# Kernel optimization log

Hardware: AMD Instinct MI355X
Metric: run time of the kernel (lower is better)

The kernel has to match this reference:

```python
import jax, jax.numpy as jnp
import numpy as np

DEPTH = 3
B, D, O = 8192, 1024, 1024
HR = 32            # router hidden
HE = 2 * D         # expert hidden
N_NODES = 2 ** DEPTH - 1
N_LEAVES = 2 ** DEPTH


def setup_inputs() -> dict:
    key = jax.random.key(0)
    ks = jax.random.split(key, 9)
    x = jax.random.normal(ks[0], (B, D), dtype=jnp.float32)
    # decision-node router params (stacked over nodes)
    rW1 = jax.random.normal(ks[1], (N_NODES, D, HR), dtype=jnp.float32) * 0.05
    rb1 = jnp.zeros((N_NODES, HR), dtype=jnp.float32)
    rW2 = jax.random.normal(ks[2], (N_NODES, HR, 2), dtype=jnp.float32) * 0.05
    rb2 = jnp.zeros((N_NODES, 2), dtype=jnp.float32)
    # leaf-expert params (stacked over experts)
    eW1 = jax.random.normal(ks[3], (N_LEAVES, D, HE), dtype=jnp.float32) * 0.02
    eb1 = jnp.zeros((N_LEAVES, HE), dtype=jnp.float32)
    eW2 = jax.random.normal(ks[4], (N_LEAVES, HE, O), dtype=jnp.float32) * 0.02
    eb2 = jnp.zeros((N_LEAVES, O), dtype=jnp.float32)
    return {"x": x, "rW1": rW1, "rb1": rb1, "rW2": rW2, "rb2": rb2,
            "eW1": eW1, "eb1": eb1, "eW2": eW2, "eb2": eb2, "top_k": 4}


def _gelu(v):
    return jax.nn.gelu(v, approximate=False)  # torch nn.GELU default = exact erf


def _leaf_probs(x, rW1, rb1, rW2, rb2):
    # all decision nodes batched: [N, B, 2]
    h = _gelu(jnp.einsum('bd,ndh->nbh', x, rW1) + rb1[:, None, :])
    logits = jnp.einsum('nbh,nhc->nbc', h, rW2) + rb2[:, None, :]
    dec = jax.nn.softmax(logits, axis=-1)
    # BFS product of path probabilities, level by level (fixed small loop)
    probs = jnp.ones((x.shape[0], 1), dtype=x.dtype)
    start = 0
    for level in range(DEPTH):
        w = 2 ** level
        dl = dec[start:start + w].transpose(1, 0, 2)       # [B, w, 2]
        probs = (probs[:, :, None] * dl).reshape(x.shape[0], 2 * w)
        start += w
    return probs  # [B, N_LEAVES]


def reference(x, rW1, rb1, rW2, rb2, eW1, eb1, eW2, eb2, top_k):
    leaf_probs = _leaf_probs(x, rW1, rb1, rW2, rb2)
    if top_k is not None and top_k < N_LEAVES:
        vals, idx = jax.lax.top_k(leaf_probs, top_k)       # [B, k]
        sparse = jnp.zeros_like(leaf_probs)
        sparse = sparse.at[jnp.arange(leaf_probs.shape[0])[:, None], idx].set(vals)
        leaf_probs = sparse / (sparse.sum(axis=1, keepdims=True) + 1e-8)
    # all leaf experts, batched (dense weighted sum; skip heuristic is an approximation)
    h = _gelu(jnp.einsum('bd,edh->ebh', x, eW1) + eb1[:, None, :])   # [E, B, HE]
    out = jnp.einsum('ebh,eho->ebo', h, eW2) + eb2[:, None, :]        # [E, B, O]
    y = jnp.einsum('ebo,be->bo', out, leaf_probs)
    return (y, leaf_probs)
```

## Files before the change

### kernel.cpp

```cpp
#include <hip/hip_runtime.h>
#include <hip/hip_bf16.h>
#include <cstdint>

#define B_   8192
#define D_   1024
#define O_   1024
#define HE_  2048
#define NN_  7
#define NL_  8
#define HR_  32
#define RC_  224
#define K3_  3072
#define MTMAX_ 264

typedef __attribute__((ext_vector_type(2))) float f32x2;
typedef __attribute__((ext_vector_type(4))) float f32x4;
typedef __attribute__((ext_vector_type(8))) short bf16x8;
typedef __attribute__((ext_vector_type(4))) unsigned short u16x4;
typedef unsigned short u16;
typedef unsigned int u32;

__device__ __forceinline__ u16 f2bf(float f) {
  __hip_bfloat16 h = __float2bfloat16(f);
  return *reinterpret_cast<u16*>(&h);
}
__device__ __forceinline__ float bf2f(u16 u) {
  u32 v = ((u32)u) << 16;
  return *reinterpret_cast<float*>(&v);
}
__device__ __forceinline__ float gelu_exact(float v) {
  return 0.5f * v * (1.0f + erff(v * 0.7071067811865475f));
}
__device__ __forceinline__ void gload16(const void* g, void* l) {
  __builtin_amdgcn_global_load_lds(
      (const __attribute__((address_space(1))) void*)(uintptr_t)g,
      (__attribute__((address_space(3))) void*)(uintptr_t)l,
      16, 0, 0);
}

__global__ __launch_bounds__(256) void build_xbs_kernel(
    const float* __restrict__ in, u16* __restrict__ out) {
  size_t i = ((size_t)blockIdx.x * 256 + threadIdx.x) * 4;
  size_t row = i >> 10;
  int col = (int)(i & 1023);
  f32x4 f = *reinterpret_cast<const f32x4*>(in + i);
  u16x4 hi, lo;
#pragma unroll
  for (int j = 0; j < 4; j++) {
    hi[j] = f2bf(f[j]);
    lo[j] = f2bf(f[j] - bf2f(hi[j]));
  }
  u16* base = out + row * 2048 + col;
  *reinterpret_cast<u16x4*>(base)        = hi;
  *reinterpret_cast<u16x4*>(base + 1024) = lo;
}

__global__ __launch_bounds__(256) void build_wr3_kernel(
    const float* __restrict__ rW1, u16* __restrict__ Wr3) {
  size_t i = ((size_t)blockIdx.x * 256 + threadIdx.x) * 4;
  int c = (int)(i / K3_), k = (int)(i % K3_);
  int j = k >> 10, kk = k & 1023;
  u16x4 o;
  if (c < RC_) {
    int node = c >> 5, h = c & 31;
    const float* src = rW1 + ((size_t)node * 1024 + kk) * HR_ + h;
#pragma unroll
    for (int t = 0; t < 4; t++) {
      float f = src[t * HR_];
      u16 hi = f2bf(f);
      o[t] = (j == 1) ? f2bf(f - bf2f(hi)) : hi;
    }
  } else {
    o[0] = 0; o[1] = 0; o[2] = 0; o[3] = 0;
  }
  *reinterpret_cast<u16x4*>(Wr3 + i) = o;
}

__global__ __launch_bounds__(256) void transpose_cvt_kernel(
    const float* __restrict__ in, u16* __restrict__ out,
    int R, int C, int ldo, long in_estride, long out_estride) {
  __shared__ __attribute__((aligned(16))) float tile[64][65];
  const float* in_e = in + (long)blockIdx.z * in_estride;
  u16* out_e = out + (long)blockIdx.z * out_estride;
  int t = threadIdx.x;
  int r0 = blockIdx.y * 64, c0 = blockIdx.x * 64;
  int cc = t & 63, rbase = t >> 6;
#pragma unroll
  for (int i = 0; i < 16; i++) {
    int rr = rbase + i * 4;
    tile[rr][cc] = in_e[(long)(r0 + rr) * C + c0 + cc];
  }
  __syncthreads();
  int r2 = (t & 31) * 2, cj = t >> 5;
#pragma unroll
  for (int i = 0; i < 8; i++) {
    int c = cj * 8 + i;
    u32 u = (u32)f2bf(tile[r2][c]) | ((u32)f2bf(tile[r2 + 1][c]) << 16);
    *reinterpret_cast<u32*>(out_e + (long)(c0 + c) * ldo + r0 + r2) = u;
  }
}

__global__ __launch_bounds__(256, 2) void router_gemm_kernel(
    const u16* __restrict__ Xbs, const u16* __restrict__ Bm,
    float* __restrict__ H1p) {
  __shared__ __attribute__((aligned(16))) u16 lA[128 * 32];
  __shared__ __attribute__((aligned(16))) u16 lB[128 * 32];
  int tid = threadIdx.x;
  int gid = blockIdx.x;
  int cpx = gridDim.x >> 3;
  gid = (gid & 7) * cpx + (gid >> 3);
  int s = gid >> 7;
  int rem = gid & 127;
  int band = rem >> 4, inb = rem & 15;
  long m0 = (long)(band * 8 + (inb & 7)) * 128;
  long n0 = (long)(inb >> 3) * 128;
  int wid = tid >> 6, lane = tid & 63;
  int wm = wid >> 1, wn = wid & 1;
  f32x4 acc[4][4];
#pragma unroll
  for (int m = 0; m < 4; m++)
#pragma unroll
    for (int n = 0; n < 4; n++) acc[m][n] = (f32x4){0.f, 0.f, 0.f, 0.f};
  int lr = lane & 15, lk = (lane >> 4) * 8;
  int srow = tid >> 2, soff = (tid & 3) * 8;
  const u16* Bb = Bm + n0 * K3_;
  int kbeg = s * 768, kend = kbeg + 768;
  for (int k0 = kbeg; k0 < kend; k0 += 32) {
    int ca = (k0 < 1024) ? k0 : k0 - 1024;
    gload16(Xbs + (m0 + srow) * 2048 + ca + soff, &lA[tid * 8]);
    gload16(Xbs + (m0 + 64 + srow) * 2048 + ca + soff, &lA[(256 + tid) * 8]);
    gload16(Bb + (long)srow * K3_ + k0 + soff, &lB[tid * 8]);
    gload16(Bb + (long)(64 + srow) * K3_ + k0 + soff, &lB[(256 + tid) * 8]);
    __syncthreads();
    bf16x8 af[4], bfr[4];
#pragma unroll
    for (int m = 0; m < 4; m++)
      af[m] = *reinterpret_cast<const bf16x8*>(&lA[(wm * 64 + m * 16 + lr) * 32 + lk]);
#pragma unroll
    for (int n = 0; n < 4; n++)
      bfr[n] = *reinterpret_cast<const bf16x8*>(&lB[(wn * 64 + n * 16 + lr) * 32 + lk]);
#pragma unroll
    for (int m = 0; m < 4; m++)
#pragma unroll
      for (int n = 0; n < 4; n++)
        acc[m][n] = __builtin_amdgcn_mfma_f32_16x16x32_bf16(af[m], bfr[n], acc[m][n], 0, 0, 0);
    __syncthreads();
  }
  int lq = lane >> 4;
#pragma unroll
  for (int m = 0; m < 4; m++)
#pragma unroll
    for (int n = 0; n < 4; n++)
#pragma unroll
      for (int j = 0; j < 4; j++) {
        long row = m0 + wm * 64 + m * 16 + lq * 4 + j;
        long col = n0 + wn * 64 + n * 16 + lr;
        if (col < RC_)
          H1p[((long)s * B_ + row) * RC_ + col] = acc[m][n][j];
      }
}

__global__ __launch_bounds__(256) void router_logits_kernel(
    const float* __restrict__ H1p, const float* __restrict__ rb1,
    const float* __restrict__ rW2, const float* __restrict__ rb2,
    const int* __restrict__ topk_ptr, float* __restrict__ P) {
  int b = blockIdx.x * 256 + threadIdx.x;
  float dec[NN_][2];
#pragma unroll
  for (int n = 0; n < NN_; n++) {
    float l0 = rb2[n * 2], l1 = rb2[n * 2 + 1];
#pragma unroll
    for (int r4 = 0; r4 < HR_; r4 += 4) {
      int c = n * HR_ + r4;
      f32x4 hs = *reinterpret_cast<const f32x4*>(&H1p[((long)0 * B_ + b) * RC_ + c]);
#pragma unroll
      for (int s = 1; s < 4; s++)
        hs += *reinterpret_cast<const f32x4*>(&H1p[((long)s * B_ + b) * RC_ + c]);
      f32x4 bv = *reinterpret_cast<const f32x4*>(rb1 + c);
#pragma unroll
      for (int j = 0; j < 4; j++) {
        float hv = gelu_exact(hs[j] + bv[j]);
        l0 += hv * rW2[(c + j) * 2];
        l1 += hv * rW2[(c + j) * 2 + 1];
      }
    }
    float mx = fmaxf(l0, l1);
    float e0 = expf(l0 - mx), e1 = expf(l1 - mx);
    float sm = e0 + e1;
    dec[n][0] = e0 / sm; dec[n][1] = e1 / sm;
  }
  float v[NL_];
#pragma unroll
  for (int L = 0; L < NL_; L++)
    v[L] = dec[0][L >> 2] * dec[1 + (L >> 2)][(L >> 1) & 1] * dec[3 + (L >> 1)][L & 1];
  int tk = *topk_ptr;
  float p[NL_];
  if (tk < NL_) {
    float s = 0.f;
    bool keep[NL_];
#pragma unroll
    for (int e = 0; e < NL_; e++) {
      int rank = 0;
#pragma unroll
      for (int j = 0; j < NL_; j++)
        rank += ((v[j] > v[e]) || (v[j] == v[e] && j < e)) ? 1 : 0;
      keep[e] = rank < tk;
      if (keep[e]) s += v[e];
    }
    float inv = 1.f / (s + 1e-8f);
#pragma unroll
    for (int e = 0; e < NL_; e++) p[e] = keep[e] ? v[e] * inv : 0.f;
  } else {
#pragma unroll
    for (int e = 0; e < NL_; e++) p[e] = v[e];
  }
#pragma unroll
  for (int e = 0; e < NL_; e++) P[(long)b * NL_ + e] = p[e];
}

__global__ __launch_bounds__(256) void yinit_kernel(
    const float* __restrict__ P, const float* __restrict__ eb2,
    float* __restrict__ y) {
  size_t i = ((size_t)blockIdx.x * 256 + threadIdx.x) * 4;
  size_t row = i >> 10;
  int col = (int)(i & 1023);
  f32x4 s = (f32x4){0.f, 0.f, 0.f, 0.f};
#pragma unroll
  for (int e = 0; e < NL_; e++) {
    float pe = P[row * NL_ + e];
    f32x4 w = *reinterpret_cast<const f32x4*>(eb2 + (size_t)e * O_ + col);
    s += w * pe;
  }
  *reinterpret_cast<f32x4*>(y + i) = s;
}

__global__ __launch_bounds__(256) void compact_kernel(
    const float* __restrict__ P, int* __restrict__ idx,
    int* __restrict__ counts) {
  int e = blockIdx.x, t = threadIdx.x;
  __shared__ int sc[256];
  __shared__ int sbase;
  if (t == 0) sbase = 0;
  __syncthreads();
  for (int c0 = 0; c0 < B_; c0 += 256) {
    int r = c0 + t;
    int f = (P[(long)r * NL_ + e] > 0.f) ? 1 : 0;
    sc[t] = f;
    __syncthreads();
#pragma unroll
    for (int d = 1; d < 256; d <<= 1) {
      int v = (t >= d) ? sc[t - d] : 0;
      __syncthreads();
      sc[t] += v;
      __syncthreads();
    }
    int pos = sbase + sc[t] - 1;
    int tot = sc[255];
    if (f) idx[(long)e * B_ + pos] = r;
    __syncthreads();
    if (t == 0) sbase += tot;
    __syncthreads();
  }
  if (t == 0) counts[e] = sbase;
}

__global__ void tiles_kernel(const int* __restrict__ counts,
                             int* __restrict__ toff) {
  int s = 0;
#pragma unroll
  for (int e = 0; e < NL_; e++) { toff[e] = s; s += (counts[e] + 127) >> 7; }
  toff[NL_] = s;
}

__global__ __launch_bounds__(256, 2) void gemme1_kernel(
    const u16* __restrict__ Xbs, const u16* __restrict__ W1t,
    const float* __restrict__ eb1, const float* __restrict__ P,
    u16* __restrict__ Hall, const int* __restrict__ idx,
    const int* __restrict__ counts, const int* __restrict__ toff) {
  __shared__ __attribute__((aligned(16))) u16 lA[128 * 32];
  __shared__ __attribute__((aligned(16))) u16 lB[128 * 32];
  int tid = threadIdx.x;
  int gid = blockIdx.x;
  int cpx = gridDim.x >> 3;
  gid = (gid & 7) * cpx + (gid >> 3);
  int mt = gid >> 4, nt = gid & 15;
  if (mt >= toff[NL_]) return;
  int e = 0;
#pragma unroll
  for (int f = 1; f < NL_; f++) e += (mt >= toff[f]) ? 1 : 0;
  int cnt = counts[e];
  long m0 = (long)(mt - toff[e]) * 128;
  long n0 = (long)nt * 128;
  const int* idxe = idx + (long)e * B_;
  int wid = tid >> 6, lane = tid & 63;
  int wm = wid >> 1, wn = wid & 1;
  f32x4 acc[4][4];
#pragma unroll
  for (int m = 0; m < 4; m++)
#pragma unroll
    for (int n = 0; n < 4; n++) acc[m][n] = (f32x4){0.f, 0.f, 0.f, 0.f};
  int lr = lane & 15, lk = (lane >> 4) * 8;
  int srow = tid >> 2, soff = (tid & 3) * 8;
  int gi0 = (m0 + srow < cnt) ? idxe[m0 + srow] : 0;
  int gi1 = (m0 + 64 + srow < cnt) ? idxe[m0 + 64 + srow] : 0;
  const u16* ar0 = Xbs + (long)gi0 * 2048;
  const u16* ar1 = Xbs + (long)gi1 * 2048;
  const u16* Bb = W1t + ((size_t)e * HE_ + n0) * D_;
  for (int k0 = 0; k0 < D_; k0 += 32) {
    gload16(ar0 + k0 + soff, &lA[tid * 8]);
    gload16(ar1 + k0 + soff, &lA[(256 + tid) * 8]);
    gload16(Bb + (long)srow * D_ + k0 + soff, &lB[tid * 8]);
    gload16(Bb + (long)(64 + srow) * D_ + k0 + soff, &lB[(256 + tid) * 8]);
    __syncthreads();
    bf16x8 af[4], bfr[4];
#pragma unroll
    for (int m = 0; m < 4; m++)
      af[m] = *reinterpret_cast<const bf16x8*>(&lA[(wm * 64 + m * 16 + lr) * 32 + lk]);
#pragma unroll
    for (int n = 0; n < 4; n++)
      bfr[n] = *reinterpret_cast<const bf16x8*>(&lB[(wn * 64 + n * 16 + lr) * 32 + lk]);
#pragma unroll
    for (int m = 0; m < 4; m++)
#pragma unroll
      for (int n = 0; n < 4; n++)
        acc[m][n] = __builtin_amdgcn_mfma_f32_16x16x32_bf16(af[m], bfr[n], acc[m][n], 0, 0, 0);
    __syncthreads();
  }
  int lq = lane >> 4;
  long hbase = (long)toff[e] * 128;
#pragma unroll
  for (int m = 0; m < 4; m++) {
#pragma unroll
    for (int j = 0; j < 4; j++) {
      long lrow = m0 + wm * 64 + m * 16 + lq * 4 + j;
      if (lrow >= cnt) continue;
      int orow = idxe[lrow];
      float pw = P[(long)orow * NL_ + e];
#pragma unroll
      for (int n = 0; n < 4; n++) {
        long col = n0 + wn * 64 + n * 16 + lr;
        float g = gelu_exact(acc[m][n][j] + eb1[(size_t)e * HE_ + col]);
        Hall[(hbase + lrow) * HE_ + col] = f2bf(g * pw);
      }
    }
  }
}

__global__ __launch_bounds__(256, 2) void gemme2_kernel(
    const u16* __restrict__ Hall, const u16* __restrict__ W2t,
    float* __restrict__ y, const int* __restrict__ idx,
    const int* __restrict__ counts, const int* __restrict__ toff) {
  __shared__ __attribute__((aligned(16))) u16 lA[128 * 32];
  __shared__ __attribute__((aligned(16))) u16 lB[128 * 32];
  int tid = threadIdx.x;
  int gid = blockIdx.x;
  int cpx = gridDim.x >> 3;
  gid = (gid & 7) * cpx + (gid >> 3);
  int mt = gid >> 3, nt = gid & 7;
  if (mt >= toff[NL_]) return;
  int e = 0;
#pragma unroll
  for (int f = 1; f < NL_; f++) e += (mt >= toff[f]) ? 1 : 0;
  int cnt = counts[e];
  long m0 = (long)(mt - toff[e]) * 128;
  long n0 = (long)nt * 128;
  const int* idxe = idx + (long)e * B_;
  int wid = tid >> 6, lane = tid & 63;
  int wm = wid >> 1, wn = wid & 1;
  f32x4 acc[4][4];
#pragma unroll
  for (int m = 0; m < 4; m++)
#pragma unroll
    for (int n = 0; n < 4; n++) acc[m][n] = (f32x4){0.f, 0.f, 0.f, 0.f};
  int lr = lane & 15, lk = (lane >> 4) * 8;
  int srow = tid >> 2, soff = (tid & 3) * 8;
  const u16* Ab = Hall + ((long)toff[e] * 128 + m0) * HE_;
  const u16* Bb = W2t + n0 * ((size_t)NL_ * HE_) + (size_t)e * HE_;
  for (int k0 = 0; k0 < HE_; k0 += 32) {
    gload16(Ab + (long)srow * HE_ + k0 + soff, &lA[tid * 8]);
    gload16(Ab + (long)(64 + srow) * HE_ + k0 + soff, &lA[(256 + tid) * 8]);
    gload16(Bb + (size_t)srow * (NL_ * HE_) + k0 + soff, &lB[tid * 8]);
    gload16(Bb + (size_t)(64 + srow) * (NL_ * HE_) + k0 + soff, &lB[(256 + tid) * 8]);
    __syncthreads();
    bf16x8 af[4], bfr[4];
#pragma unroll
    for (int m = 0; m < 4; m++)
      af[m] = *reinterpret_cast<const bf16x8*>(&lA[(wm * 64 + m * 16 + lr) * 32 + lk]);
#pragma unroll
    for (int n = 0; n < 4; n++)
      bfr[n] = *reinterpret_cast<const bf16x8*>(&lB[(wn * 64 + n * 16 + lr) * 32 + lk]);
#pragma unroll
    for (int m = 0; m < 4; m++)
#pragma unroll
      for (int n = 0; n < 4; n++)
        acc[m][n] = __builtin_amdgcn_mfma_f32_16x16x32_bf16(af[m], bfr[n], acc[m][n], 0, 0, 0);
    __syncthreads();
  }
  int lq = lane >> 4;
#pragma unroll
  for (int m = 0; m < 4; m++) {
#pragma unroll
    for (int j = 0; j < 4; j++) {
      long lrow = m0 + wm * 64 + m * 16 + lq * 4 + j;
      if (lrow >= cnt) continue;
      long orow = idxe[lrow];
#pragma unroll
      for (int n = 0; n < 4; n++) {
        long col = n0 + wn * 64 + n * 16 + lr;
        unsafeAtomicAdd(&y[orow * O_ + col], acc[m][n][j]);
      }
    }
  }
}

extern "C" void kernel_launch(void* const* d_in, const int* in_sizes, int n_in,
                              void* d_out, int out_size, void* d_ws, size_t ws_size,
                              hipStream_t stream) {
  (void)in_sizes; (void)n_in; (void)out_size; (void)ws_size;
  const float* x   = (const float*)d_in[0];
  const float* rW1 = (const float*)d_in[1];
  const float* rb1 = (const float*)d_in[2];
  const float* rW2 = (const float*)d_in[3];
  const float* rb2 = (const float*)d_in[4];
  const float* eW1 = (const float*)d_in[5];
  const float* eb1 = (const float*)d_in[6];
  const float* eW2 = (const float*)d_in[7];
  const float* eb2 = (const float*)d_in[8];
  const int*  topk = (const int*)d_in[9];
  float* y = (float*)d_out;
  float* P = y + (size_t)B_ * O_;

  char* ws = (char*)d_ws;
  u16*  Xbs = (u16*)ws;
  u16*  W1t = (u16*)(ws + 33554432);
  u16*  W2t = (u16*)(ws + 67108864);
  int*  idx    = (int*)(ws + 100663296);
  int*  counts = (int*)(ws + 100925440);
  int*  toff   = (int*)(ws + 100925504);
  char* hreg   = ws + 100925952;
  u16*  Hall = (u16*)hreg;
  u16*  Wr3  = (u16*)hreg;
  float* H1p = (float*)(hreg + 2097152);

  build_xbs_kernel<<<(B_ * D_) / 1024, 256, 0, stream>>>(x, Xbs);
  build_wr3_kernel<<<(256 * K3_) / 1024, 256, 0, stream>>>(rW1, Wr3);
  transpose_cvt_kernel<<<dim3(HE_ / 64, D_ / 64, NL_), 256, 0, stream>>>(
      eW1, W1t, D_, HE_, D_, (long)D_ * HE_, (long)HE_ * D_);
  transpose_cvt_kernel<<<dim3(O_ / 64, HE_ / 64, NL_), 256, 0, stream>>>(
      eW2, W2t, HE_, O_, NL_ * HE_, (long)HE_ * O_, (long)HE_);
  router_gemm_kernel<<<512, 256, 0, stream>>>(Xbs, Wr3, H1p);
  router_logits_kernel<<<B_ / 256, 256, 0, stream>>>(H1p, rb1, rW2, rb2, topk, P);
  yinit_kernel<<<(B_ * O_) / 1024, 256, 0, stream>>>(P, eb2, y);
  compact_kernel<<<NL_, 256, 0, stream>>>(P, idx, counts);
  tiles_kernel<<<1, 1, 0, stream>>>(counts, toff);

  gemme1_kernel<<<MTMAX_ * 16, 256, 0, stream>>>(
      Xbs, W1t, eb1, P, Hall, idx, counts, toff);
  gemme2_kernel<<<MTMAX_ * 8, 256, 0, stream>>>(
      Hall, W2t, y, idx, counts, toff);
}
```

Measured before the change: 721.8 us.

## Deepen expert GEMM K-tile to 64 with XOR-swizzled LDS and per-expert W2 layout

```diff
diff --git a/kernel.cpp b/kernel.cpp
--- a/kernel.cpp
+++ b/kernel.cpp
@@ -277,8 +277,8 @@
     const float* __restrict__ eb1, const float* __restrict__ P,
     u16* __restrict__ Hall, const int* __restrict__ idx,
     const int* __restrict__ counts, const int* __restrict__ toff) {
-  __shared__ __attribute__((aligned(16))) u16 lA[128 * 32];
-  __shared__ __attribute__((aligned(16))) u16 lB[128 * 32];
+  __shared__ __attribute__((aligned(16))) u16 lA[128 * 64];
+  __shared__ __attribute__((aligned(16))) u16 lB[128 * 64];
   int tid = threadIdx.x;
   int gid = blockIdx.x;
   int cpx = gridDim.x >> 3;
@@ -299,31 +299,60 @@
   for (int m = 0; m < 4; m++)
 #pragma unroll
     for (int n = 0; n < 4; n++) acc[m][n] = (f32x4){0.f, 0.f, 0.f, 0.f};
-  int lr = lane & 15, lk = (lane >> 4) * 8;
-  int srow = tid >> 2, soff = (tid & 3) * 8;
-  int gi0 = (m0 + srow < cnt) ? idxe[m0 + srow] : 0;
-  int gi1 = (m0 + 64 + srow < cnt) ? idxe[m0 + 64 + srow] : 0;
-  const u16* ar0 = Xbs + (long)gi0 * 2048;
-  const u16* ar1 = Xbs + (long)gi1 * 2048;
+  int lr = lane & 15, lkg = lane >> 4;
+  const u16* gA[4]; const u16* gB[4]; int lds_o[4];
   const u16* Bb = W1t + ((size_t)e * HE_ + n0) * D_;
-  for (int k0 = 0; k0 < D_; k0 += 32) {
-    gload16(ar0 + k0 + soff, &lA[tid * 8]);
-    gload16(ar1 + k0 + soff, &lA[(256 + tid) * 8]);
-    gload16(Bb + (long)srow * D_ + k0 + soff, &lB[tid * 8]);
-    gload16(Bb + (long)(64 + srow) * D_ + k0 + soff, &lB[(256 + tid) * 8]);
-    __syncthreads();
-    bf16x8 af[4], bfr[4];
+#pragma unroll
+  for (int i = 0; i < 4; i++) {
+    int sidx = tid + i * 256;
+    int r = sidx >> 3, j = sidx & 7;
+    int so = ((j ^ (r & 7)) << 3);
+    int gi = (m0 + r < cnt) ? idxe[m0 + r] : 0;
+    gA[i] = Xbs + (long)gi * 2048 + so;
+    gB[i] = Bb + (long)r * D_ + so;
+    lds_o[i] = sidx * 8;
+  }
+  int foA[4][2], foB[4][2];
+#pragma unroll
+  for (int m = 0; m < 4; m++) {
+    int r = wm * 64 + m * 16 + lr;
+#pragma unroll
+    for (int kk = 0; kk < 2; kk++)
+      foA[m][kk] = r * 128 + ((((kk * 4 + lkg) ^ (r & 7))) << 4);
+  }
+#pragma unroll
+  for (int n = 0; n < 4; n++) {
+    int r = wn * 64 + n * 16 + lr;
+#pragma unroll
+    for (int kk = 0; kk < 2; kk++)
+      foB[n][kk] = r * 128 + ((((kk * 4 + lkg) ^ (r & 7))) << 4);
+  }
+  const char* pa = (const char*)lA;
+  const char* pb = (const char*)lB;
+  for (int k0 = 0; k0 < D_; k0 += 64) {
+#pragma unroll
+    for (int i = 0; i < 4; i++) gload16(gA[i] + k0, &lA[lds_o[i]]);
+#pragma unroll
+    for (int i = 0; i < 4; i++) gload16(gB[i] + k0, &lB[lds_o[i]]);
+    __syncthreads();
+    bf16x8 af[4][2], bfr[4][2];
+#pragma unroll
+    for (int m = 0; m < 4; m++) {
+      af[m][0] = *reinterpret_cast<const bf16x8*>(pa + foA[m][0]);
+      af[m][1] = *reinterpret_cast<const bf16x8*>(pa + foA[m][1]);
+    }
+#pragma unroll
+    for (int n = 0; n < 4; n++) {
+      bfr[n][0] = *reinterpret_cast<const bf16x8*>(pb + foB[n][0]);
+      bfr[n][1] = *reinterpret_cast<const bf16x8*>(pb + foB[n][1]);
+    }
 #pragma unroll
     for (int m = 0; m < 4; m++)
-      af[m] = *reinterpret_cast<const bf16x8*>(&lA[(wm * 64 + m * 16 + lr) * 32 + lk]);
-#pragma unroll
-    for (int n = 0; n < 4; n++)
-      bfr[n] = *reinterpret_cast<const bf16x8*>(&lB[(wn * 64 + n * 16 + lr) * 32 + lk]);
-#pragma unroll
-    for (int m = 0; m < 4; m++)
-#pragma unroll
-      for (int n = 0; n < 4; n++)
-        acc[m][n] = __builtin_amdgcn_mfma_f32_16x16x32_bf16(af[m], bfr[n], acc[m][n], 0, 0, 0);
+#pragma unroll
+      for (int n = 0; n < 4; n++) {
+        acc[m][n] = __builtin_amdgcn_mfma_f32_16x16x32_bf16(af[m][0], bfr[n][0], acc[m][n], 0, 0, 0);
+        acc[m][n] = __builtin_amdgcn_mfma_f32_16x16x32_bf16(af[m][1], bfr[n][1], acc[m][n], 0, 0, 0);
+      }
     __syncthreads();
   }
   int lq = lane >> 4;
@@ -350,8 +379,8 @@
     const u16* __restrict__ Hall, const u16* __restrict__ W2t,
     float* __restrict__ y, const int* __restrict__ idx,
     const int* __restrict__ counts, const int* __restrict__ toff) {
-  __shared__ __attribute__((aligned(16))) u16 lA[128 * 32];
-  __shared__ __attribute__((aligned(16))) u16 lB[128 * 32];
+  __shared__ __attribute__((aligned(16))) u16 lA[128 * 64];
+  __shared__ __attribute__((aligned(16))) u16 lB[128 * 64];
   int tid = threadIdx.x;
   int gid = blockIdx.x;
   int cpx = gridDim.x >> 3;
@@ -372,28 +401,60 @@
   for (int m = 0; m < 4; m++)
 #pragma unroll
     for (int n = 0; n < 4; n++) acc[m][n] = (f32x4){0.f, 0.f, 0.f, 0.f};
-  int lr = lane & 15, lk = (lane >> 4) * 8;
-  int srow = tid >> 2, soff = (tid & 3) * 8;
+  int lr = lane & 15, lkg = lane >> 4;
   const u16* Ab = Hall + ((long)toff[e] * 128 + m0) * HE_;
-  const u16* Bb = W2t + n0 * ((size_t)NL_ * HE_) + (size_t)e * HE_;
-  for (int k0 = 0; k0 < HE_; k0 += 32) {
-    gload16(Ab + (long)srow * HE_ + k0 + soff, &lA[tid * 8]);
-    gload16(Ab + (long)(64 + srow) * HE_ + k0 + soff, &lA[(256 + tid) * 8]);
-    gload16(Bb + (size_t)srow * (NL_ * HE_) + k0 + soff, &lB[tid * 8]);
-    gload16(Bb + (size_t)(64 + srow) * (NL_ * HE_) + k0 + soff, &lB[(256 + tid) * 8]);
-    __syncthreads();
-    bf16x8 af[4], bfr[4];
+  const u16* Bb = W2t + ((size_t)e * O_ + n0) * HE_;
+  const u16* gA[4]; const u16* gB[4]; int lds_o[4];
+#pragma unroll
+  for (int i = 0; i < 4; i++) {
+    int sidx = tid + i * 256;
+    int r = sidx >> 3, j = sidx & 7;
+    int so = ((j ^ (r & 7)) << 3);
+    gA[i] = Ab + (long)r * HE_ + so;
+    gB[i] = Bb + (long)r * HE_ + so;
+    lds_o[i] = sidx * 8;
+  }
+  int foA[4][2], foB[4][2];
+#pragma unroll
+  for (int m = 0; m < 4; m++) {
+    int r = wm * 64 + m * 16 + lr;
+#pragma unroll
+    for (int kk = 0; kk < 2; kk++)
+      foA[m][kk] = r * 128 + ((((kk * 4 + lkg) ^ (r & 7))) << 4);
+  }
+#pragma unroll
+  for (int n = 0; n < 4; n++) {
+    int r = wn * 64 + n * 16 + lr;
+#pragma unroll
+    for (int kk = 0; kk < 2; kk++)
+      foB[n][kk] = r * 128 + ((((kk * 4 + lkg) ^ (r & 7))) << 4);
+  }
+  const char* pa = (const char*)lA;
+  const char* pb = (const char*)lB;
+  for (int k0 = 0; k0 < HE_; k0 += 64) {
+#pragma unroll
+    for (int i = 0; i < 4; i++) gload16(gA[i] + k0, &lA[lds_o[i]]);
+#pragma unroll
+    for (int i = 0; i < 4; i++) gload16(gB[i] + k0, &lB[lds_o[i]]);
+    __syncthreads();
+    bf16x8 af[4][2], bfr[4][2];
+#pragma unroll
+    for (int m = 0; m < 4; m++) {
+      af[m][0] = *reinterpret_cast<const bf16x8*>(pa + foA[m][0]);
+      af[m][1] = *reinterpret_cast<const bf16x8*>(pa + foA[m][1]);
+    }
+#pragma unroll
+    for (int n = 0; n < 4; n++) {
+      bfr[n][0] = *reinterpret_cast<const bf16x8*>(pb + foB[n][0]);
+      bfr[n][1] = *reinterpret_cast<const bf16x8*>(pb + foB[n][1]);
+    }
 #pragma unroll
     for (int m = 0; m < 4; m++)
-      af[m] = *reinterpret_cast<const bf16x8*>(&lA[(wm * 64 + m * 16 + lr) * 32 + lk]);
-#pragma unroll
-    for (int n = 0; n < 4; n++)
-      bfr[n] = *reinterpret_cast<const bf16x8*>(&lB[(wn * 64 + n * 16 + lr) * 32 + lk]);
-#pragma unroll
-    for (int m = 0; m < 4; m++)
-#pragma unroll
-      for (int n = 0; n < 4; n++)
-        acc[m][n] = __builtin_amdgcn_mfma_f32_16x16x32_bf16(af[m], bfr[n], acc[m][n], 0, 0, 0);
+#pragma unroll
+      for (int n = 0; n < 4; n++) {
+        acc[m][n] = __builtin_amdgcn_mfma_f32_16x16x32_bf16(af[m][0], bfr[n][0], acc[m][n], 0, 0, 0);
+        acc[m][n] = __builtin_amdgcn_mfma_f32_16x16x32_bf16(af[m][1], bfr[n][1], acc[m][n], 0, 0, 0);
+      }
     __syncthreads();
   }
   int lq = lane >> 4;
@@ -447,7 +508,7 @@
   transpose_cvt_kernel<<<dim3(HE_ / 64, D_ / 64, NL_), 256, 0, stream>>>(
       eW1, W1t, D_, HE_, D_, (long)D_ * HE_, (long)HE_ * D_);
   transpose_cvt_kernel<<<dim3(O_ / 64, HE_ / 64, NL_), 256, 0, stream>>>(
-      eW2, W2t, HE_, O_, NL_ * HE_, (long)HE_ * O_, (long)HE_);
+      eW2, W2t, HE_, O_, HE_, (long)HE_ * O_, (long)O_ * HE_);
   router_gemm_kernel<<<512, 256, 0, stream>>>(Xbs, Wr3, H1p);
   router_logits_kernel<<<B_ / 256, 256, 0, stream>>>(H1p, rb1, rW2, rb2, topk, P);
   yinit_kernel<<<(B_ * O_) / 1024, 256, 0, stream>>>(P, eb2, y);
```

Result: faster. 669.6 us (-7.2%).
